# Kernel tuning notes

Hardware: AMD Instinct MI355X
Metric: run time of the kernel (lower is better)

## Reference

```python
import jax, jax.numpy as jnp
import numpy as np

B, C, CI, H, W = 4, 128, 64, 96, 96  # batch, in_channels, inter_channels, spatial
SS = 2                                # sub_sample_factor (maxpool on phi and g)
BN_EPS = 1e-5


def conv1x1(x, w, b):
    # x: [B,C,H,W], w: [O,C], b: [O]
    return jnp.einsum('bchw,oc->bohw', x, w) + b[None, :, None, None]


def maxpool2(x):
    # 2x2 max pool, stride 2. x: [B,C,H,W]
    b, c, h, w = x.shape
    return x.reshape(b, c, h // 2, 2, w // 2, 2).max(axis=(3, 5))


def setup_inputs() -> dict:
    key = jax.random.key(0)
    ks = jax.random.split(key, 12)
    s_in = 1.0 / np.sqrt(C)
    s_ci = 1.0 / np.sqrt(CI)
    return {
        'x':        jax.random.normal(ks[0], (B, C, H, W), jnp.float32),
        'g_w':      jax.random.normal(ks[1], (CI, C), jnp.float32) * s_in,
        'g_b':      jax.random.normal(ks[2], (CI,), jnp.float32) * 0.01,
        'theta_w':  jax.random.normal(ks[3], (CI, C), jnp.float32) * s_in,
        'theta_b':  jax.random.normal(ks[4], (CI,), jnp.float32) * 0.01,
        'phi_w':    jax.random.normal(ks[5], (CI, C), jnp.float32) * s_in,
        'phi_b':    jax.random.normal(ks[6], (CI,), jnp.float32) * 0.01,
        'W_w':      jax.random.normal(ks[7], (C, CI), jnp.float32) * s_ci,
        'W_b':      jax.random.normal(ks[8], (C,), jnp.float32) * 0.01,
        'bn_gamma': jax.random.normal(ks[9], (C,), jnp.float32) * 0.1 + 1.0,
        'bn_beta':  jax.random.normal(ks[10], (C,), jnp.float32) * 0.1,
        'bn_mean':  jax.random.normal(ks[11], (C,), jnp.float32) * 0.1,
        'bn_var':   jax.random.uniform(jax.random.fold_in(key, 99), (C,), jnp.float32, 0.5, 1.5),
    }


def reference(x, g_w, g_b, theta_w, theta_b, phi_w, phi_b, W_w, W_b,
              bn_gamma, bn_beta, bn_mean, bn_var):
    b = x.shape[0]
    # g: conv1x1 -> maxpool(2) -> [B, N_kv, CI]
    g_x = maxpool2(conv1x1(x, g_w, g_b)).reshape(b, CI, -1).transpose(0, 2, 1)
    # theta: conv1x1 -> [B, N_q, CI]
    theta_x = conv1x1(x, theta_w, theta_b).reshape(b, CI, -1).transpose(0, 2, 1)
    # phi: conv1x1 -> maxpool(2) -> [B, CI, N_kv]
    phi_x = maxpool2(conv1x1(x, phi_w, phi_b)).reshape(b, CI, -1)
    # full affinity [B, N_q, N_kv], softmax over keys (embedded_gaussian)
    f = jnp.einsum('bqc,bck->bqk', theta_x, phi_x)
    attn = jax.nn.softmax(f, axis=-1)
    y = jnp.einsum('bqk,bkc->bqc', attn, g_x)            # [B, N_q, CI]
    y = y.transpose(0, 2, 1).reshape(b, CI, H, W)
    # W: conv1x1 (CI -> C) + BatchNorm (inference form) + residual
    W_y = conv1x1(y, W_w, W_b)
    inv = bn_gamma * jax.lax.rsqrt(bn_var + BN_EPS)
    W_y = W_y * inv[None, :, None, None] + (bn_beta - bn_mean * inv)[None, :, None, None]
    return W_y + x
```

## Files before the change

kernel.cpp:

```cpp
#include <hip/hip_runtime.h>
#include <hip/hip_bf16.h>

#define NB 4
#define NC 128
#define NH 96
#define NQ 9216
#define NKV 2304

typedef __bf16 bf8 __attribute__((ext_vector_type(8)));
typedef float f4 __attribute__((ext_vector_type(4)));
typedef unsigned short u16t;
typedef unsigned int u32t;
typedef u32t u32x4 __attribute__((ext_vector_type(4)));
typedef u16t u16x4v __attribute__((ext_vector_type(4)));

static __device__ __forceinline__ u16t f2bf(float f){
  u32t u = __builtin_bit_cast(u32t, f);
  u = (u + 0x7fffu + ((u >> 16) & 1u)) >> 16;
  return (u16t)u;
}

static __device__ __forceinline__ f4 mfma16(bf8 a, bf8 b, f4 c){
  return __builtin_amdgcn_mfma_f32_16x16x32_bf16(a, b, c, 0, 0, 0);
}

#define GLDS16(gp, lp) __builtin_amdgcn_global_load_lds( \
    (const u32t*)(gp), (u32t*)(lp), 16, 0, 0)

__global__ __launch_bounds__(256) void prep_weights(
    const float* __restrict__ g_w, const float* __restrict__ theta_w,
    const float* __restrict__ phi_w, const float* __restrict__ W_w,
    const float* __restrict__ W_b, const float* __restrict__ bn_gamma,
    const float* __restrict__ bn_beta, const float* __restrict__ bn_mean,
    const float* __restrict__ bn_var,
    u16t* __restrict__ wt_theta, u16t* __restrict__ wt_phi,
    u16t* __restrict__ wt_g, u16t* __restrict__ wt_W,
    float* __restrict__ alpha, float* __restrict__ beta2)
{
  int i = blockIdx.x * 256 + threadIdx.x;
  wt_theta[i] = f2bf(theta_w[i]);
  wt_phi[i]   = f2bf(phi_w[i]);
  wt_g[i]     = f2bf(g_w[i]);
  wt_W[i]     = f2bf(W_w[i]);
  if (blockIdx.x == 0 && threadIdx.x < 128){
    int t = threadIdx.x;
    float inv = bn_gamma[t] * rsqrtf(bn_var[t] + 1e-5f);
    alpha[t] = inv;
    beta2[t] = W_b[t]*inv + bn_beta[t] - bn_mean[t]*inv;
  }
}

__global__ __launch_bounds__(256) void conv3_pool(
    const float* __restrict__ x,
    const u16t* __restrict__ wt_theta, const u16t* __restrict__ wt_phi,
    const u16t* __restrict__ wt_g,
    const float* __restrict__ theta_b, const float* __restrict__ phi_b,
    const float* __restrict__ g_b,
    u16t* __restrict__ theta, u16t* __restrict__ phi, u16t* __restrict__ g_t)
{
  __shared__ __align__(16) u16t xt[64][136];
  const int blk = blockIdx.x;
  const int batch = blk / 144;
  const int t144 = blk % 144;
  const int ph = t144 / 3;
  const int pw0 = (t144 % 3) * 16;
  const int t = threadIdx.x;
  const float* xb = x + (size_t)batch * NC * NQ;

  #pragma unroll
  for (int i = 0; i < 8; ++i){
    int slot = i*256 + t;
    int c = slot >> 4;
    int quad = slot & 15;
    int row = quad >> 3, col4 = (quad & 7)*4;
    int q = (ph*2 + row)*NH + pw0*2 + col4;
    float4 v = *(const float4*)&xb[(size_t)c*NQ + q];
    int pl = row*32 + col4;
    xt[pl+0][c] = f2bf(v.x);
    xt[pl+1][c] = f2bf(v.y);
    xt[pl+2][c] = f2bf(v.z);
    xt[pl+3][c] = f2bf(v.w);
  }
  __syncthreads();

  const int w = t >> 6, l = t & 63, lm = l & 15, lg = l >> 4;
  auto PL = [](int pxi){
    return (((pxi>>1)&1) << 5) + 8*(pxi>>4) + 2*((pxi>>2)&3) + (pxi&1);
  };
  auto QROW = [&](int pxi){
    return (ph*2 + ((pxi>>1)&1))*NH + (pw0 + 4*(pxi>>4) + ((pxi>>2)&3))*2 + (pxi&1);
  };
  bf8 a[4];
  #pragma unroll
  for (int k = 0; k < 4; ++k)
    a[k] = *(const bf8*)&xt[PL(w*16 + lm)][k*32 + lg*8];

  const int kvbase = ph*48 + pw0;
  const int kv = kvbase + 4*w + lg;

  f4 Dth[4];
  #pragma unroll
  for (int s = 0; s < 4; ++s){
    float bv = theta_b[s*16 + lm];
    f4 D = {bv, bv, bv, bv};
    #pragma unroll
    for (int k = 0; k < 4; ++k){
      bf8 b = *(const bf8*)&wt_theta[(s*16 + lm)*128 + k*32 + lg*8];
      D = mfma16(a[k], b, D);
    }
    Dth[s] = D;
  }
  {
    u16t* pp = phi + (size_t)batch * NKV * 64;
    #pragma unroll
    for (int s = 0; s < 4; ++s){
      float bv = phi_b[s*16 + lm];
      f4 D = {bv, bv, bv, bv};
      #pragma unroll
      for (int k = 0; k < 4; ++k){
        bf8 b = *(const bf8*)&wt_phi[(s*16 + lm)*128 + k*32 + lg*8];
        D = mfma16(a[k], b, D);
      }
      float mx = fmaxf(fmaxf(D[0], D[1]), fmaxf(D[2], D[3]));
      pp[(size_t)kv*64 + s*16 + lm] = f2bf(mx);
    }
  }
  float gmx[4];
  #pragma unroll
  for (int s = 0; s < 4; ++s){
    float bv = g_b[s*16 + lm];
    f4 D = {bv, bv, bv, bv};
    #pragma unroll
    for (int k = 0; k < 4; ++k){
      bf8 b = *(const bf8*)&wt_g[(s*16 + lm)*128 + k*32 + lg*8];
      D = mfma16(a[k], b, D);
    }
    gmx[s] = fmaxf(fmaxf(D[0], D[1]), fmaxf(D[2], D[3]));
  }

  __syncthreads();
  u16t* tl = &xt[0][0];
  u16t* gl = &xt[0][0] + 4608;
  #pragma unroll
  for (int s = 0; s < 4; ++s){
    #pragma unroll
    for (int r = 0; r < 4; ++r)
      tl[(w*16 + lg*4 + r)*72 + s*16 + lm] = f2bf(Dth[s][r]);
    gl[(s*16 + lm)*20 + 4*w + lg] = f2bf(gmx[s]);
  }
  __syncthreads();
  {
    u16t* th = theta + (size_t)batch * NQ * 64;
    #pragma unroll
    for (int p = 0; p < 2; ++p){
      int slot = t + 256*p;
      int row = slot >> 3, piece = slot & 7;
      int q = QROW(row);
      *(bf8*)&th[(size_t)q*64 + piece*8] = *(const bf8*)&tl[row*72 + piece*8];
    }
  }
  {
    u16t* gt = g_t + (size_t)batch * 64 * NKV;
    int c = t >> 2, L = t & 3;
    int T = (kvbase >> 4) & 3;
    int kvg = kvbase & ~63;
    u16x4v v;
    #pragma unroll
    for (int u = 0; u < 4; ++u) v[u] = gl[c*20 + L*4 + u];
    *(u16x4v*)&gt[(size_t)c*NKV + kvg + (T>>1)*32 + ((T&1)<<2) + L*8] = v;
  }
}

#define PHI_OFF 0
#define G_OFF   49152
#define SCRAP_OFF 98304
#define Y_OFF   76800

__global__ __launch_bounds__(384) void attn_fused(
    const u16t* __restrict__ theta, const u16t* __restrict__ phi,
    const u16t* __restrict__ g_t, const u16t* __restrict__ wt_W,
    const float* __restrict__ alpha, const float* __restrict__ beta2,
    const float* __restrict__ x, float* __restrict__ out)
{
  __shared__ __align__(16) char SM[102400];
  __shared__ float sums[2][144];

  const int bid = blockIdx.x;
  const int blk = (bid & 7)*32 + (bid >> 3);
  const int batch = blk >> 6;
  const int qb = (blk & 63) * 144;
  const int t = threadIdx.x;
  const int w = t >> 6, l = t & 63, lm = l & 15, lg = l >> 4;
  const int qw = w >> 1, kh = w & 1;

  const u16t* th = theta + ((size_t)batch*NQ + qb)*64;
  bf8 a[3][2];
  #pragma unroll
  for (int mr = 0; mr < 3; ++mr){
    a[mr][0] = *(const bf8*)&th[(qw*48 + mr*16 + lm)*64 + lg*8];
    a[mr][1] = *(const bf8*)&th[(qw*48 + mr*16 + lm)*64 + 32 + lg*8];
  }
  asm volatile("s_waitcnt vmcnt(0)" ::: "memory");

  const char* phc = (const char*)(phi + (size_t)batch*NKV*64);
  const char* gtc = (const char*)(g_t + (size_t)batch*64*NKV);

  auto STAGE = [&](int kt_s, int bufc){
    #pragma unroll
    for (int j = 0; j < 6; ++j){
      int u = w*6 + j;
      int ur = (u < 32) ? u : (u - 32);
      int khu = ur >> 4, isg = (ur >> 3) & 1, sub = ur & 7;
      int row = sub*8 + (l >> 3);
      int swz = ((l & 7) ^ (l >> 3)) << 4;
      int kb = (khu*18 + kt_s) * 64;
      char* dst = (u < 32)
        ? SM + (isg ? G_OFF : PHI_OFF) + (khu*3 + bufc)*8192 + sub*1024 + l*16
        : SM + SCRAP_OFF + (u - 32)*1024 + l*16;
      const char* src = isg
        ? gtc + (size_t)row*(NKV*2) + (size_t)kb*2 + swz
        : phc + (size_t)(kb + row)*128 + swz;
      GLDS16(src, dst);
    }
  };

  f4 Y[3][4];
  #pragma unroll
  for (int mr = 0; mr < 3; ++mr)
    #pragma unroll
    for (int s = 0; s < 4; ++s)
      Y[mr][s] = f4{0.f, 0.f, 0.f, 0.f};
  float lsum[3] = {0.f, 0.f, 0.f};

  STAGE(0, 0);
  STAGE(1, 1);

  int bufc = 0;
  for (int kt = 0; kt < 18; ++kt){
    __builtin_amdgcn_s_barrier();
    if (kt < 16){
      STAGE(kt + 2, (bufc == 0) ? 2 : bufc - 1);
      asm volatile("s_waitcnt vmcnt(12)" ::: "memory");
    } else if (kt == 16){
      asm volatile("s_waitcnt vmcnt(6)" ::: "memory");
    } else {
      asm volatile("s_waitcnt vmcnt(0)" ::: "memory");
    }
    __builtin_amdgcn_s_barrier();

    const char* pb = SM + PHI_OFF + (kh*3 + bufc)*8192;
    const char* gb = SM + G_OFF   + (kh*3 + bufc)*8192;
    const int m7 = lm & 7;

    bf8 bp[4][2];
    #pragma unroll
    for (int tt = 0; tt < 4; ++tt){
      int rb = (tt*16 + lm)*128;
      bp[tt][0] = *(const bf8*)(pb + rb + ((lg ^ m7) << 4));
      bp[tt][1] = *(const bf8*)(pb + rb + (((4 + lg) ^ m7) << 4));
    }
    bf8 bg[4][2];
    #pragma unroll
    for (int s = 0; s < 4; ++s){
      int rb = (s*16 + lm)*128;
      bg[s][0] = *(const bf8*)(gb + rb + ((lg ^ m7) << 4));
      bg[s][1] = *(const bf8*)(gb + rb + (((4 + lg) ^ m7) << 4));
    }

    #pragma unroll
    for (int mr = 0; mr < 3; ++mr){
      f4 S[4];
      __builtin_amdgcn_s_setprio(1);
      #pragma unroll
      for (int tt = 0; tt < 4; ++tt){
        f4 z = {0.f, 0.f, 0.f, 0.f};
        z = mfma16(bp[tt][0], a[mr][0], z);
        S[tt] = mfma16(bp[tt][1], a[mr][1], z);
      }
      __builtin_amdgcn_s_setprio(0);
      u32t wq[8];
      #pragma unroll
      for (int tt = 0; tt < 4; ++tt){
        float p0, p1, p2, p3;
        float a0 = fmaf(S[tt][0], 1.44269504f, -43.2808512f);
        float a1 = fmaf(S[tt][1], 1.44269504f, -43.2808512f);
        float a2 = fmaf(S[tt][2], 1.44269504f, -43.2808512f);
        float a3 = fmaf(S[tt][3], 1.44269504f, -43.2808512f);
        asm("v_exp_f32 %0, %1" : "=v"(p0) : "v"(a0));
        asm("v_exp_f32 %0, %1" : "=v"(p1) : "v"(a1));
        asm("v_exp_f32 %0, %1" : "=v"(p2) : "v"(a2));
        asm("v_exp_f32 %0, %1" : "=v"(p3) : "v"(a3));
        lsum[mr] += (p0 + p1) + (p2 + p3);
        asm("v_cvt_pk_bf16_f32 %0, %1, %2" : "=v"(wq[tt*2])   : "v"(p0), "v"(p1));
        asm("v_cvt_pk_bf16_f32 %0, %1, %2" : "=v"(wq[tt*2+1]) : "v"(p2), "v"(p3));
      }
      bf8 pa0 = __builtin_bit_cast(bf8, u32x4{wq[0], wq[1], wq[2], wq[3]});
      bf8 pa1 = __builtin_bit_cast(bf8, u32x4{wq[4], wq[5], wq[6], wq[7]});
      __builtin_amdgcn_s_setprio(1);
      #pragma unroll
      for (int s = 0; s < 4; ++s){
        Y[mr][s] = mfma16(pa0, bg[s][0], Y[mr][s]);
        Y[mr][s] = mfma16(pa1, bg[s][1], Y[mr][s]);
      }
      __builtin_amdgcn_s_setprio(0);
    }
    bufc = (bufc == 2) ? 0 : bufc + 1;
  }

  #pragma unroll
  for (int mr = 0; mr < 3; ++mr){
    float sv = lsum[mr];
    sv += __shfl_xor(sv, 16);
    sv += __shfl_xor(sv, 32);
    if (lg == 0) sums[kh][qw*48 + mr*16 + lm] = sv;
  }

  __syncthreads();
  float (*yp)[68] = (float (*)[68])SM;
  if (kh == 0){
    #pragma unroll
    for (int mr = 0; mr < 3; ++mr)
      #pragma unroll
      for (int s = 0; s < 4; ++s)
        #pragma unroll
        for (int r = 0; r < 4; ++r)
          yp[qw*48 + mr*16 + lg*4 + r][s*16 + lm] = Y[mr][s][r];
  }
  __syncthreads();
  if (kh == 1){
    #pragma unroll
    for (int mr = 0; mr < 3; ++mr)
      #pragma unroll
      for (int s = 0; s < 4; ++s)
        #pragma unroll
        for (int r = 0; r < 4; ++r)
          yp[qw*48 + mr*16 + lg*4 + r][s*16 + lm] += Y[mr][s][r];
  }
  __syncthreads();

  u16t* yl = (u16t*)(SM + Y_OFF);
  #pragma unroll
  for (int i = 0; i < 12; ++i){
    int p = t + 384*i;
    int q = p >> 5, cp = p & 31;
    float tot = sums[0][q] + sums[1][q];
    float inv = 1.0f / tot;
    float v0 = yp[q][cp*2] * inv;
    float v1 = yp[q][cp*2 + 1] * inv;
    u32t pk;
    asm("v_cvt_pk_bf16_f32 %0, %1, %2" : "=v"(pk) : "v"(v0), "v"(v1));
    *(u32t*)&yl[q*72 + cp*2] = pk;
  }
  __syncthreads();

  float (*ol)[130] = (float (*)[130])SM;
  #pragma unroll
  for (int i = 0; i < 12; ++i){
    int tau = w + 6*i;
    int qt = tau >> 3, ct = tau & 7;
    bf8 ya0 = *(const bf8*)&yl[(qt*16 + lm)*72 + lg*8];
    bf8 ya1 = *(const bf8*)&yl[(qt*16 + lm)*72 + 32 + lg*8];
    const u16t* wr = wt_W + (ct*16 + lm)*64;
    bf8 b0 = *(const bf8*)&wr[lg*8];
    bf8 b1 = *(const bf8*)&wr[lg*8 + 32];
    f4 z = {0.f, 0.f, 0.f, 0.f};
    z = mfma16(ya0, b0, z);
    z = mfma16(ya1, b1, z);
    #pragma unroll
    for (int r = 0; r < 4; ++r)
      ol[qt*16 + lg*4 + r][ct*16 + lm] = z[r];
  }
  __syncthreads();

  const float* xb = x + (size_t)batch*NC*NQ + qb;
  float* ob = out + (size_t)batch*NC*NQ + qb;
  #pragma unroll
  for (int i = 0; i < 12; ++i){
    int idx = t + 384*i;
    int c = idx / 36, qv = idx % 36;
    float4 xv = *(const float4*)&xb[(size_t)c*NQ + qv*4];
    float al = alpha[c], be = beta2[c];
    float4 ov;
    ov.x = ol[qv*4 + 0][c]*al + be + xv.x;
    ov.y = ol[qv*4 + 1][c]*al + be + xv.y;
    ov.z = ol[qv*4 + 2][c]*al + be + xv.z;
    ov.w = ol[qv*4 + 3][c]*al + be + xv.w;
    *(float4*)&ob[(size_t)c*NQ + qv*4] = ov;
  }
}

extern "C" void kernel_launch(void* const* d_in, const int* in_sizes, int n_in,
                              void* d_out, int out_size, void* d_ws, size_t ws_size,
                              hipStream_t stream)
{
  const float* x       = (const float*)d_in[0];
  const float* g_w     = (const float*)d_in[1];
  const float* g_b     = (const float*)d_in[2];
  const float* theta_w = (const float*)d_in[3];
  const float* theta_b = (const float*)d_in[4];
  const float* phi_w   = (const float*)d_in[5];
  const float* phi_b   = (const float*)d_in[6];
  const float* W_w     = (const float*)d_in[7];
  const float* W_b     = (const float*)d_in[8];
  const float* bn_g    = (const float*)d_in[9];
  const float* bn_b    = (const float*)d_in[10];
  const float* bn_m    = (const float*)d_in[11];
  const float* bn_v    = (const float*)d_in[12];
  float* out = (float*)d_out;

  char* ws = (char*)d_ws;
  size_t off = 0;
  u16t* theta = (u16t*)(ws + off); off += (size_t)NB*NQ*64*2;
  u16t* phi   = (u16t*)(ws + off); off += (size_t)NB*NKV*64*2;
  u16t* g_t   = (u16t*)(ws + off); off += (size_t)NB*64*NKV*2;
  u16t* wt_theta = (u16t*)(ws + off); off += 64*128*2;
  u16t* wt_phi   = (u16t*)(ws + off); off += 64*128*2;
  u16t* wt_g     = (u16t*)(ws + off); off += 64*128*2;
  u16t* wt_W     = (u16t*)(ws + off); off += 128*64*2;
  float* alpha = (float*)(ws + off); off += 128*4;
  float* beta2 = (float*)(ws + off); off += 128*4;
  if (off > ws_size) return;

  prep_weights<<<32, 256, 0, stream>>>(g_w, theta_w, phi_w, W_w, W_b,
                                       bn_g, bn_b, bn_m, bn_v,
                                       wt_theta, wt_phi, wt_g, wt_W, alpha, beta2);
  conv3_pool<<<576, 256, 0, stream>>>(x, wt_theta, wt_phi, wt_g,
                                      theta_b, phi_b, g_b, theta, phi, g_t);
  attn_fused<<<256, 384, 0, stream>>>(theta, phi, g_t, wt_W, alpha, beta2, x, out);
}
```

Before: 77.73 us.

## Split attention KV range across four waves per query group with 768-thread blocks

```diff
diff --git a/kernel.cpp b/kernel.cpp
--- a/kernel.cpp
+++ b/kernel.cpp
@@ -172,18 +172,16 @@
 }
 
 #define PHI_OFF 0
-#define G_OFF   49152
-#define SCRAP_OFF 98304
-#define Y_OFF   76800
-
-__global__ __launch_bounds__(384) void attn_fused(
+#define G_OFF   65536
+#define SCRAP_OFF 131072
+
+__global__ __launch_bounds__(768) void attn_fused(
     const u16t* __restrict__ theta, const u16t* __restrict__ phi,
     const u16t* __restrict__ g_t, const u16t* __restrict__ wt_W,
     const float* __restrict__ alpha, const float* __restrict__ beta2,
     const float* __restrict__ x, float* __restrict__ out)
 {
-  __shared__ __align__(16) char SM[102400];
-  __shared__ float sums[2][144];
+  __shared__ __align__(16) char SM[139264];
 
   const int bid = blockIdx.x;
   const int blk = (bid & 7)*32 + (bid >> 3);
@@ -191,7 +189,7 @@
   const int qb = (blk & 63) * 144;
   const int t = threadIdx.x;
   const int w = t >> 6, l = t & 63, lm = l & 15, lg = l >> 4;
-  const int qw = w >> 1, kh = w & 1;
+  const int qw = w >> 2, kh = w & 3;
 
   const u16t* th = theta + ((size_t)batch*NQ + qb)*64;
   bf8 a[3][2];
@@ -209,14 +207,14 @@
     #pragma unroll
     for (int j = 0; j < 6; ++j){
       int u = w*6 + j;
-      int ur = (u < 32) ? u : (u - 32);
+      int ur = (u < 64) ? u : (u - 64);
       int khu = ur >> 4, isg = (ur >> 3) & 1, sub = ur & 7;
       int row = sub*8 + (l >> 3);
       int swz = ((l & 7) ^ (l >> 3)) << 4;
-      int kb = (khu*18 + kt_s) * 64;
-      char* dst = (u < 32)
-        ? SM + (isg ? G_OFF : PHI_OFF) + (khu*3 + bufc)*8192 + sub*1024 + l*16
-        : SM + SCRAP_OFF + (u - 32)*1024 + l*16;
+      int kb = (khu*9 + kt_s) * 64;
+      char* dst = (u < 64)
+        ? SM + (isg ? G_OFF : PHI_OFF) + (khu*2 + bufc)*8192 + sub*1024 + l*16
+        : SM + SCRAP_OFF + (u - 64)*1024 + l*16;
       const char* src = isg
         ? gtc + (size_t)row*(NKV*2) + (size_t)kb*2 + swz
         : phc + (size_t)(kb + row)*128 + swz;
@@ -225,31 +223,32 @@
   };
 
   f4 Y[3][4];
-  #pragma unroll
-  for (int mr = 0; mr < 3; ++mr)
+  f4 Ysum[3];
+  #pragma unroll
+  for (int mr = 0; mr < 3; ++mr){
     #pragma unroll
     for (int s = 0; s < 4; ++s)
       Y[mr][s] = f4{0.f, 0.f, 0.f, 0.f};
-  float lsum[3] = {0.f, 0.f, 0.f};
+    Ysum[mr] = f4{0.f, 0.f, 0.f, 0.f};
+  }
+  const u32t ONE2 = 0x3f803f80u;
+  const bf8 vones = __builtin_bit_cast(bf8, u32x4{ONE2, ONE2, ONE2, ONE2});
 
   STAGE(0, 0);
-  STAGE(1, 1);
-
-  int bufc = 0;
-  for (int kt = 0; kt < 18; ++kt){
+
+  for (int kt = 0; kt < 9; ++kt){
+    const int buf = kt & 1;
     __builtin_amdgcn_s_barrier();
-    if (kt < 16){
-      STAGE(kt + 2, (bufc == 0) ? 2 : bufc - 1);
-      asm volatile("s_waitcnt vmcnt(12)" ::: "memory");
-    } else if (kt == 16){
+    if (kt < 8){
+      STAGE(kt + 1, buf ^ 1);
       asm volatile("s_waitcnt vmcnt(6)" ::: "memory");
     } else {
       asm volatile("s_waitcnt vmcnt(0)" ::: "memory");
     }
     __builtin_amdgcn_s_barrier();
 
-    const char* pb = SM + PHI_OFF + (kh*3 + bufc)*8192;
-    const char* gb = SM + G_OFF   + (kh*3 + bufc)*8192;
+    const char* pb = SM + PHI_OFF + (kh*2 + buf)*8192;
+    const char* gb = SM + G_OFF   + (kh*2 + buf)*8192;
     const int m7 = lm & 7;
 
     bf8 bp[4][2];
@@ -270,14 +269,12 @@
     #pragma unroll
     for (int mr = 0; mr < 3; ++mr){
       f4 S[4];
-      __builtin_amdgcn_s_setprio(1);
       #pragma unroll
       for (int tt = 0; tt < 4; ++tt){
         f4 z = {0.f, 0.f, 0.f, 0.f};
         z = mfma16(bp[tt][0], a[mr][0], z);
         S[tt] = mfma16(bp[tt][1], a[mr][1], z);
       }
-      __builtin_amdgcn_s_setprio(0);
       u32t wq[8];
       #pragma unroll
       for (int tt = 0; tt < 4; ++tt){
@@ -290,73 +287,78 @@
         asm("v_exp_f32 %0, %1" : "=v"(p1) : "v"(a1));
         asm("v_exp_f32 %0, %1" : "=v"(p2) : "v"(a2));
         asm("v_exp_f32 %0, %1" : "=v"(p3) : "v"(a3));
-        lsum[mr] += (p0 + p1) + (p2 + p3);
         asm("v_cvt_pk_bf16_f32 %0, %1, %2" : "=v"(wq[tt*2])   : "v"(p0), "v"(p1));
         asm("v_cvt_pk_bf16_f32 %0, %1, %2" : "=v"(wq[tt*2+1]) : "v"(p2), "v"(p3));
       }
       bf8 pa0 = __builtin_bit_cast(bf8, u32x4{wq[0], wq[1], wq[2], wq[3]});
       bf8 pa1 = __builtin_bit_cast(bf8, u32x4{wq[4], wq[5], wq[6], wq[7]});
-      __builtin_amdgcn_s_setprio(1);
       #pragma unroll
       for (int s = 0; s < 4; ++s){
         Y[mr][s] = mfma16(pa0, bg[s][0], Y[mr][s]);
         Y[mr][s] = mfma16(pa1, bg[s][1], Y[mr][s]);
       }
-      __builtin_amdgcn_s_setprio(0);
-    }
-    bufc = (bufc == 2) ? 0 : bufc + 1;
-  }
-
-  #pragma unroll
-  for (int mr = 0; mr < 3; ++mr){
-    float sv = lsum[mr];
-    sv += __shfl_xor(sv, 16);
-    sv += __shfl_xor(sv, 32);
-    if (lg == 0) sums[kh][qw*48 + mr*16 + lm] = sv;
-  }
-
-  __syncthreads();
-  float (*yp)[68] = (float (*)[68])SM;
-  if (kh == 0){
-    #pragma unroll
-    for (int mr = 0; mr < 3; ++mr)
+      Ysum[mr] = mfma16(pa0, vones, Ysum[mr]);
+      Ysum[mr] = mfma16(pa1, vones, Ysum[mr]);
+    }
+  }
+
+  __syncthreads();
+  float (*ypA)[68] = (float (*)[68])SM;
+  float (*ypB)[68] = (float (*)[68])(SM + 39168);
+  float (*myp)[68] = (kh < 2) ? ypA : ypB;
+
+  if ((kh & 1) == 0){
+    #pragma unroll
+    for (int mr = 0; mr < 3; ++mr){
       #pragma unroll
       for (int s = 0; s < 4; ++s)
         #pragma unroll
         for (int r = 0; r < 4; ++r)
-          yp[qw*48 + mr*16 + lg*4 + r][s*16 + lm] = Y[mr][s][r];
-  }
-  __syncthreads();
-  if (kh == 1){
-    #pragma unroll
-    for (int mr = 0; mr < 3; ++mr)
+          myp[qw*48 + mr*16 + lg*4 + r][s*16 + lm] = Y[mr][s][r];
+      if (lm == 0){
+        #pragma unroll
+        for (int r = 0; r < 4; ++r)
+          myp[qw*48 + mr*16 + lg*4 + r][64] = Ysum[mr][r];
+      }
+    }
+  }
+  __syncthreads();
+  if ((kh & 1) == 1){
+    #pragma unroll
+    for (int mr = 0; mr < 3; ++mr){
       #pragma unroll
       for (int s = 0; s < 4; ++s)
         #pragma unroll
         for (int r = 0; r < 4; ++r)
-          yp[qw*48 + mr*16 + lg*4 + r][s*16 + lm] += Y[mr][s][r];
-  }
-  __syncthreads();
-
-  u16t* yl = (u16t*)(SM + Y_OFF);
-  #pragma unroll
-  for (int i = 0; i < 12; ++i){
-    int p = t + 384*i;
+          myp[qw*48 + mr*16 + lg*4 + r][s*16 + lm] += Y[mr][s][r];
+      if (lm == 0){
+        #pragma unroll
+        for (int r = 0; r < 4; ++r)
+          myp[qw*48 + mr*16 + lg*4 + r][64] += Ysum[mr][r];
+      }
+    }
+  }
+  __syncthreads();
+
+  u16t* yl = (u16t*)(SM + 78336);
+  #pragma unroll
+  for (int i = 0; i < 6; ++i){
+    int p = t + 768*i;
     int q = p >> 5, cp = p & 31;
-    float tot = sums[0][q] + sums[1][q];
+    float tot = ypA[q][64] + ypB[q][64];
     float inv = 1.0f / tot;
-    float v0 = yp[q][cp*2] * inv;
-    float v1 = yp[q][cp*2 + 1] * inv;
+    float v0 = (ypA[q][cp*2]     + ypB[q][cp*2])     * inv;
+    float v1 = (ypA[q][cp*2 + 1] + ypB[q][cp*2 + 1]) * inv;
     u32t pk;
     asm("v_cvt_pk_bf16_f32 %0, %1, %2" : "=v"(pk) : "v"(v0), "v"(v1));
     *(u32t*)&yl[q*72 + cp*2] = pk;
   }
   __syncthreads();
 
-  float (*ol)[130] = (float (*)[130])SM;
-  #pragma unroll
-  for (int i = 0; i < 12; ++i){
-    int tau = w + 6*i;
+  float (*ol)[131] = (float (*)[131])SM;
+  #pragma unroll
+  for (int i = 0; i < 6; ++i){
+    int tau = w + 12*i;
     int qt = tau >> 3, ct = tau & 7;
     bf8 ya0 = *(const bf8*)&yl[(qt*16 + lm)*72 + lg*8];
     bf8 ya1 = *(const bf8*)&yl[(qt*16 + lm)*72 + 32 + lg*8];
@@ -375,8 +377,8 @@
   const float* xb = x + (size_t)batch*NC*NQ + qb;
   float* ob = out + (size_t)batch*NC*NQ + qb;
   #pragma unroll
-  for (int i = 0; i < 12; ++i){
-    int idx = t + 384*i;
+  for (int i = 0; i < 6; ++i){
+    int idx = t + 768*i;
     int c = idx / 36, qv = idx % 36;
     float4 xv = *(const float4*)&xb[(size_t)c*NQ + qv*4];
     float al = alpha[c], be = beta2[c];
@@ -426,5 +428,5 @@
                                        wt_theta, wt_phi, wt_g, wt_W, alpha, beta2);
   conv3_pool<<<576, 256, 0, stream>>>(x, wt_theta, wt_phi, wt_g,
                                       theta_b, phi_b, g_b, theta, phi, g_t);
-  attn_fused<<<256, 384, 0, stream>>>(theta, phi, g_t, wt_W, alpha, beta2, x, out);
-}
+  attn_fused<<<256, 768, 0, stream>>>(theta, phi, g_t, wt_W, alpha, beta2, x, out);
+}
```

Measured after the change: 97.84 us. 1.26x slower.
